# Performance work log

Hardware: AMD Instinct MI355X
Metric: run time of the kernel (lower is better)

## Reference

```python
import jax, jax.numpy as jnp
import numpy as np

DIM = 768
HEADS = 12
HEAD_DIM = DIM // HEADS
SCALE = HEAD_DIM ** -0.5


def setup_inputs() -> dict:
    key = jax.random.key(0)
    k1, k2, k3, k4 = jax.random.split(key, 4)
    x = jax.random.normal(k1, (8, 1025, DIM), dtype=jnp.float32)
    # torch nn.Linear weight layout: (out_features, in_features)
    w_qkv = jax.random.normal(k2, (3 * DIM, DIM), dtype=jnp.float32) * (DIM ** -0.5)
    w_proj = jax.random.normal(k3, (DIM, DIM), dtype=jnp.float32) * (DIM ** -0.5)
    b_proj = jax.random.normal(k4, (DIM,), dtype=jnp.float32) * 0.01
    return {"x": x, "w_qkv": w_qkv, "w_proj": w_proj, "b_proj": b_proj}


def reference(x, w_qkv, w_proj, b_proj):
    B, N, C = x.shape
    H, D = HEADS, HEAD_DIM
    # qkv: (B, N, 3C) -> (3, B, H, N, D)
    qkv = jnp.einsum('bnc,oc->bno', x, w_qkv)
    qkv = qkv.reshape(B, N, 3, H, D).transpose(2, 0, 3, 1, 4)
    q, k, v = qkv[0], qkv[1], qkv[2]
    attn = jnp.einsum('bhnd,bhmd->bhnm', q, k) * SCALE
    attn = jax.nn.softmax(attn, axis=-1)
    out = jnp.einsum('bhnm,bhmd->bhnd', attn, v)
    out = out.transpose(0, 2, 1, 3).reshape(B, N, C)
    out = jnp.einsum('bnc,oc->bno', out, w_proj) + b_proj
    return out
```

## Files before the change

kernel.cpp:

```cpp
#include <hip/hip_runtime.h>
#include <stdint.h>

#define DIMC 768
#define NSEQ 1025
#define BATCH 8
#define HEADS 12
#define HDIM 64
#define OC3 2304
#define MROWS (BATCH * NSEQ)
#define KVB 64
#define NT 17
#define QTILE 128
#define NQT 9
#define C2 0.1803368801111244f
#define OFFB (-11.541560327111707f)

typedef short bf16x8 __attribute__((ext_vector_type(8)));
typedef float f32x4 __attribute__((ext_vector_type(4)));
typedef float f32x16 __attribute__((ext_vector_type(16)));
typedef uint32_t u32x4 __attribute__((ext_vector_type(4)));

__device__ __forceinline__ uint32_t f2bf(float x) {
    uint32_t u = __builtin_bit_cast(uint32_t, x);
    return (u + 0x7fffu + ((u >> 16) & 1u)) >> 16;
}
__device__ __forceinline__ float4 ld4(const float* p) {
    return *reinterpret_cast<const float4*>(p);
}
__device__ __forceinline__ uint32_t cvtpk(float lo, float hi) {
    uint32_t r;
    asm("v_cvt_pk_bf16_f32 %0, %1, %2" : "=v"(r) : "v"(lo), "v"(hi));
    return r;
}
__device__ __forceinline__ void plswap(uint32_t& x, uint32_t& y) {
    asm volatile("v_permlane32_swap_b32 %0, %1" : "+v"(x), "+v"(y));
}
__device__ __forceinline__ void async_cp16(void* lds, const void* g) {
    __builtin_amdgcn_global_load_lds(
        (const __attribute__((address_space(1))) uint32_t*)g,
        (__attribute__((address_space(3))) uint32_t*)lds, 16, 0, 0);
}

__global__ __launch_bounds__(256) void cvt_all(const float* __restrict__ x,
                                               const float* __restrict__ wq,
                                               const float* __restrict__ wp,
                                               uint16_t* __restrict__ xb,
                                               uint16_t* __restrict__ wqb,
                                               uint16_t* __restrict__ wpb) {
    const int NX = MROWS * DIMC / 8, NQ = OC3 * DIMC / 8, NP = DIMC * DIMC / 8;
    const int i = blockIdx.x * 256 + threadIdx.x;
    const float* src;
    uint16_t* dst;
    int off;
    if (i < NX)                { src = x;  dst = xb;  off = i; }
    else if (i < NX + NQ)      { src = wq; dst = wqb; off = i - NX; }
    else if (i < NX + NQ + NP) { src = wp; dst = wpb; off = i - NX - NQ; }
    else return;
    const float4 a = ld4(src + off * 8), b = ld4(src + off * 8 + 4);
    uint4 o;
    o.x = f2bf(a.x) | (f2bf(a.y) << 16);
    o.y = f2bf(a.z) | (f2bf(a.w) << 16);
    o.z = f2bf(b.x) | (f2bf(b.y) << 16);
    o.w = f2bf(b.z) | (f2bf(b.w) << 16);
    *reinterpret_cast<uint4*>(dst + off * 8) = o;
}

template <bool OUTBF, bool BIAS>
__global__ __launch_bounds__(256) void gemm_bf16_nt(const uint16_t* __restrict__ A,
                                                    const uint16_t* __restrict__ W,
                                                    const float* __restrict__ bias,
                                                    void* __restrict__ Out,
                                                    int M, int N, int K) {
    __shared__ __align__(16) char smem[32768];
    char* const As = smem;
    char* const Ws = smem + 16384;

    const int tid = threadIdx.x;
    const int wave = tid >> 6, lane = tid & 63;
    const int l15 = lane & 15, l4 = lane >> 4;
    const int wr = wave >> 1, wc = wave & 1;
    const int m0 = blockIdx.y * 128, n0 = blockIdx.x * 128;

    f32x4 acc[4][4] = {};

    int srow[4], scol[4];
#pragma unroll
    for (int i = 0; i < 4; ++i) {
        const int X = i * 4096 + wave * 1024 + lane * 16;
        const int row = X >> 7;
        const int slot = (X & 127) >> 4;
        srow[i] = row;
        scol[i] = (slot ^ (row & 7)) << 3;
    }

    for (int kt = 0; kt < K; kt += 64) {
        __syncthreads();
#pragma unroll
        for (int i = 0; i < 4; ++i) {
            int am = m0 + srow[i];
            if (am >= M) am = M - 1;
            async_cp16(As + i * 4096 + wave * 1024,
                       A + (size_t)am * K + kt + scol[i]);
            const int wn = n0 + srow[i];
            async_cp16(Ws + i * 4096 + wave * 1024,
                       W + (size_t)wn * K + kt + scol[i]);
        }
        __syncthreads();

#pragma unroll
        for (int ch = 0; ch < 2; ++ch) {
            const int kb = (ch << 6) + (l4 << 4);
            bf16x8 af[4], bw[4];
#pragma unroll
            for (int mi = 0; mi < 4; ++mi) {
                const int row = wr * 64 + mi * 16 + l15;
                af[mi] = *(const bf16x8*)(As + (row << 7) + (kb ^ ((row & 7) << 4)));
            }
#pragma unroll
            for (int nj = 0; nj < 4; ++nj) {
                const int row = wc * 64 + nj * 16 + l15;
                bw[nj] = *(const bf16x8*)(Ws + (row << 7) + (kb ^ ((row & 7) << 4)));
            }
#pragma unroll
            for (int mi = 0; mi < 4; ++mi)
#pragma unroll
                for (int nj = 0; nj < 4; ++nj)
                    acc[mi][nj] = __builtin_amdgcn_mfma_f32_16x16x32_bf16(
                        af[mi], bw[nj], acc[mi][nj], 0, 0, 0);
        }
    }

#pragma unroll
    for (int mi = 0; mi < 4; ++mi) {
#pragma unroll
        for (int r = 0; r < 4; ++r) {
            const int m = m0 + wr * 64 + mi * 16 + l4 * 4 + r;
            if (m < M) {
#pragma unroll
                for (int nj = 0; nj < 4; ++nj) {
                    const int n = n0 + wc * 64 + nj * 16 + l15;
                    float v = acc[mi][nj][r];
                    if (BIAS) v += bias[n];
                    if (OUTBF)
                        ((uint16_t*)Out)[(size_t)m * N + n] = (uint16_t)f2bf(v);
                    else
                        ((float*)Out)[(size_t)m * N + n] = v;
                }
            }
        }
    }
}

__global__ __launch_bounds__(256) void flash_attn2(const uint16_t* __restrict__ qkv,
                                                   uint16_t* __restrict__ out) {
    const int wg = blockIdx.x;
    const int lg = (wg & 7) * 108 + (wg >> 3);
    const int qt = lg % NQT;
    const int hb = lg / NQT;
    const int h = hb % HEADS, b = hb / HEADS;

    const int tid = threadIdx.x;
    const int wave = tid >> 6, lane = tid & 63;
    const int l31 = lane & 31, lh = lane >> 5;

    __shared__ __align__(16) char smem[32768];

    const uint16_t* Kg = qkv + (size_t)b * NSEQ * OC3 + DIMC + h * HDIM;
    const uint16_t* Vg = qkv + (size_t)b * NSEQ * OC3 + 2 * DIMC + h * HDIM;

    bf16x8 qf[4];
    {
        int qrow = qt * QTILE + wave * 32 + l31;
        if (qrow > NSEQ - 1) qrow = NSEQ - 1;
        const uint16_t* Qg = qkv + (size_t)(b * NSEQ + qrow) * OC3 + h * HDIM;
#pragma unroll
        for (int ds = 0; ds < 4; ++ds)
            qf[ds] = *(const bf16x8*)(Qg + ds * 16 + lh * 8);
    }

    bf16x8 ones;
#pragma unroll
    for (int i = 0; i < 8; ++i) ones[i] = (short)0x3F80;

    uint4 va, vb;
    const int kvp = tid & 31;
    const int vd0 = (tid >> 5) * 8;

    auto stageK = [&](int kv0, char* Kb) {
#pragma unroll
        for (int i = 0; i < 2; ++i) {
            const int X = i * 4096 + wave * 1024 + lane * 16;
            const int row = X >> 7;
            const int slot = (X & 127) >> 4;
            int kvg = kv0 + row;
            if (kvg > NSEQ - 1) kvg = NSEQ - 1;
            async_cp16(Kb + i * 4096 + wave * 1024,
                       Kg + (size_t)kvg * OC3 + ((slot ^ (row & 7)) << 3));
        }
    };
    auto loadV = [&](int kv0) {
        int ka = kv0 + kvp * 2, kb2 = ka + 1;
        if (ka > NSEQ - 1) ka = NSEQ - 1;
        if (kb2 > NSEQ - 1) kb2 = NSEQ - 1;
        va = *(const uint4*)(Vg + (size_t)ka * OC3 + vd0);
        vb = *(const uint4*)(Vg + (size_t)kb2 * OC3 + vd0);
    };
    auto writeV = [&](char* Vb) {
        const uint32_t aw[4] = {va.x, va.y, va.z, va.w};
        const uint32_t bw[4] = {vb.x, vb.y, vb.z, vb.w};
#pragma unroll
        for (int t4 = 0; t4 < 4; ++t4) {
            const uint32_t lo = __builtin_amdgcn_perm(bw[t4], aw[t4], 0x05040100u);
            const uint32_t hi = __builtin_amdgcn_perm(bw[t4], aw[t4], 0x07060302u);
            const int dl = vd0 + t4 * 2, dh = dl + 1;
            *(uint32_t*)(Vb + (((dl << 7) + (kvp << 2)) ^ ((dl & 7) << 4))) = lo;
            *(uint32_t*)(Vb + (((dh << 7) + (kvp << 2)) ^ ((dh & 7) << 4))) = hi;
        }
    };

    stageK(0, smem);
    loadV(0);
    writeV(smem + 16384);
    __syncthreads();

    f32x16 o[2] = {};
    f32x16 osum = {};

    for (int t = 0; t < NT; ++t) {
        const int cur = t & 1;
        const int kv0 = t * KVB;
        char* const Kc = smem + cur * 8192;
        char* const Vc = smem + 16384 + cur * 8192;

        if (t < NT - 1) {
            stageK(kv0 + KVB, smem + (cur ^ 1) * 8192);
            loadV(kv0 + KVB);
        }

        f32x16 s[2] = {};
        __builtin_amdgcn_s_setprio(1);
#pragma unroll
        for (int kvb = 0; kvb < 2; ++kvb) {
            const int krow = kvb * 32 + l31;
            const int kbase = (krow << 7);
            const int sw = (l31 & 7) << 4;
#pragma unroll
            for (int ds = 0; ds < 4; ++ds) {
                bf16x8 kf = *(const bf16x8*)(Kc + kbase + ((ds * 32 + lh * 16) ^ sw));
                s[kvb] = __builtin_amdgcn_mfma_f32_32x32x16_bf16(kf, qf[ds], s[kvb], 0, 0, 0);
            }
        }
        __builtin_amdgcn_s_setprio(0);

        if (t == NT - 1) {
#pragma unroll
            for (int kvb = 0; kvb < 2; ++kvb)
#pragma unroll
                for (int r = 0; r < 16; ++r) {
                    const int kvg = kv0 + kvb * 32 + (r & 3) + 8 * (r >> 2) + 4 * lh;
                    if (kvg >= NSEQ) s[kvb][r] = -INFINITY;
                }
        }

#pragma unroll
        for (int kvb = 0; kvb < 2; ++kvb)
#pragma unroll
            for (int r = 0; r < 16; ++r)
                s[kvb][r] = __builtin_amdgcn_exp2f(fmaf(s[kvb][r], C2, OFFB));

        bf16x8 pa[4];
#pragma unroll
        for (int kb = 0; kb < 4; ++kb) {
            const f32x16 S = s[kb >> 1];
            const int c = (kb & 1) * 8;
            uint32_t w0 = cvtpk(S[c + 0], S[c + 1]);
            uint32_t w2 = cvtpk(S[c + 4], S[c + 5]);
            plswap(w0, w2);
            uint32_t w1 = cvtpk(S[c + 2], S[c + 3]);
            uint32_t w3 = cvtpk(S[c + 6], S[c + 7]);
            plswap(w1, w3);
            u32x4 w;
            w[0] = w0; w[1] = w1; w[2] = w2; w[3] = w3;
            pa[kb] = __builtin_bit_cast(bf16x8, w);
        }

        __builtin_amdgcn_s_setprio(1);
#pragma unroll
        for (int kb = 0; kb < 4; ++kb)
            osum = __builtin_amdgcn_mfma_f32_32x32x16_bf16(ones, pa[kb], osum, 0, 0, 0);
#pragma unroll
        for (int db = 0; db < 2; ++db) {
            const int d = db * 32 + l31;
            const int dbase = (d << 7);
            const int sw = (l31 & 7) << 4;
#pragma unroll
            for (int kb = 0; kb < 4; ++kb) {
                bf16x8 vf = *(const bf16x8*)(Vc + dbase + ((kb * 32 + lh * 16) ^ sw));
                o[db] = __builtin_amdgcn_mfma_f32_32x32x16_bf16(vf, pa[kb], o[db], 0, 0, 0);
            }
        }
        __builtin_amdgcn_s_setprio(0);

        if (t < NT - 1) {
            writeV(smem + 16384 + (cur ^ 1) * 8192);
            __syncthreads();
        }
    }

    {
        const int qrow = qt * QTILE + wave * 32 + l31;
        if (qrow < NSEQ) {
            const float inv = 1.0f / osum[0];
            uint16_t* orow = out + (size_t)(b * NSEQ + qrow) * DIMC + h * HDIM;
#pragma unroll
            for (int db = 0; db < 2; ++db)
#pragma unroll
                for (int g = 0; g < 4; ++g) {
                    const int d = db * 32 + g * 8 + lh * 4;
                    uint2 ww;
                    ww.x = cvtpk(o[db][g * 4 + 0] * inv, o[db][g * 4 + 1] * inv);
                    ww.y = cvtpk(o[db][g * 4 + 2] * inv, o[db][g * 4 + 3] * inv);
                    *(uint2*)(orow + d) = ww;
                }
        }
    }
}

extern "C" void kernel_launch(void* const* d_in, const int* in_sizes, int n_in,
                              void* d_out, int out_size, void* d_ws, size_t ws_size,
                              hipStream_t stream) {
    const float* x      = (const float*)d_in[0];
    const float* w_qkv  = (const float*)d_in[1];
    const float* w_proj = (const float*)d_in[2];
    const float* b_proj = (const float*)d_in[3];
    float* out = (float*)d_out;

    uint16_t* xb   = (uint16_t*)d_ws;
    uint16_t* wqb  = xb  + (size_t)MROWS * DIMC;
    uint16_t* wpb  = wqb + (size_t)OC3 * DIMC;
    uint16_t* qkv  = wpb + (size_t)DIMC * DIMC;
    uint16_t* attb = qkv + (size_t)MROWS * OC3;

    const dim3 blk(256);
    const int ncvt = (MROWS * DIMC + OC3 * DIMC + DIMC * DIMC) / 8;
    cvt_all<<<dim3((ncvt + 255) / 256), blk, 0, stream>>>(x, w_qkv, w_proj, xb, wqb, wpb);

    gemm_bf16_nt<true, false><<<dim3(OC3 / 128, (MROWS + 127) / 128), blk, 0, stream>>>(
        xb, wqb, nullptr, qkv, MROWS, OC3, DIMC);

    flash_attn2<<<dim3(NQT * HEADS * BATCH), blk, 0, stream>>>(qkv, attb);

    gemm_bf16_nt<false, true><<<dim3(DIMC / 128, (MROWS + 127) / 128), blk, 0, stream>>>(
        attb, wpb, b_proj, out, MROWS, DIMC, DIMC);
}
```

Baseline: 127.6 us.

## Emit head-major Q/K and transposed V from QKV GEMM epilogue

The QKV GEMM epilogue now scatters its output into per-(batch, head) Q and K buffers and a transposed V buffer laid out [bh][d][seq], instead of one interleaved qkv matrix. The attention kernel can then stage V into shared memory with the same async 16-byte copies used for K. This removes the register load, permute and LDS write path for V and the extra sync it needed. In exchange, the epilogue issues 2-byte transposed V stores strided by 1025 elements, which coalesce poorly. The V row stride is odd, so the 16-byte async reads are misaligned, and the last tile reads past the end of each row into neighbouring data, relying on masking to discard it.

Measured after the change: 139.7 us. 9.5% more time.

```diff
diff --git a/kernel.cpp b/kernel.cpp
--- a/kernel.cpp
+++ b/kernel.cpp
@@ -8,6 +8,7 @@
 #define HDIM 64
 #define OC3 2304
 #define MROWS (BATCH * NSEQ)
+#define NBH (BATCH * HEADS)
 #define KVB 64
 #define NT 17
 #define QTILE 128
@@ -65,11 +66,14 @@
     *reinterpret_cast<uint4*>(dst + off * 8) = o;
 }
 
-template <bool OUTBF, bool BIAS>
+template <bool QKVOUT, bool BIAS>
 __global__ __launch_bounds__(256) void gemm_bf16_nt(const uint16_t* __restrict__ A,
                                                     const uint16_t* __restrict__ W,
                                                     const float* __restrict__ bias,
                                                     void* __restrict__ Out,
+                                                    uint16_t* __restrict__ qh,
+                                                    uint16_t* __restrict__ kh,
+                                                    uint16_t* __restrict__ vt,
                                                     int M, int N, int K) {
     __shared__ __align__(16) char smem[32768];
     char* const As = smem;
@@ -136,28 +140,47 @@
         for (int r = 0; r < 4; ++r) {
             const int m = m0 + wr * 64 + mi * 16 + l4 * 4 + r;
             if (m < M) {
-#pragma unroll
-                for (int nj = 0; nj < 4; ++nj) {
-                    const int n = n0 + wc * 64 + nj * 16 + l15;
-                    float v = acc[mi][nj][r];
-                    if (BIAS) v += bias[n];
-                    if (OUTBF)
-                        ((uint16_t*)Out)[(size_t)m * N + n] = (uint16_t)f2bf(v);
-                    else
+                if (QKVOUT) {
+                    const int bidx = m / NSEQ;
+                    const int nq = m - bidx * NSEQ;
+#pragma unroll
+                    for (int nj = 0; nj < 4; ++nj) {
+                        const int n = n0 + wc * 64 + nj * 16 + l15;
+                        const uint16_t v = (uint16_t)f2bf(acc[mi][nj][r]);
+                        const int part = n / DIMC;
+                        const int hh = (n - part * DIMC) >> 6;
+                        const int dd = n & 63;
+                        const size_t bh = (size_t)bidx * HEADS + hh;
+                        if (part == 0)
+                            qh[(bh * NSEQ + nq) * HDIM + dd] = v;
+                        else if (part == 1)
+                            kh[(bh * NSEQ + nq) * HDIM + dd] = v;
+                        else
+                            vt[(bh * HDIM + dd) * NSEQ + nq] = v;
+                    }
+                } else {
+#pragma unroll
+                    for (int nj = 0; nj < 4; ++nj) {
+                        const int n = n0 + wc * 64 + nj * 16 + l15;
+                        float v = acc[mi][nj][r];
+                        if (BIAS) v += bias[n];
                         ((float*)Out)[(size_t)m * N + n] = v;
+                    }
                 }
             }
         }
     }
 }
 
-__global__ __launch_bounds__(256) void flash_attn2(const uint16_t* __restrict__ qkv,
+__global__ __launch_bounds__(256) void flash_attn2(const uint16_t* __restrict__ qh,
+                                                   const uint16_t* __restrict__ kh,
+                                                   const uint16_t* __restrict__ vt,
                                                    uint16_t* __restrict__ out) {
     const int wg = blockIdx.x;
     const int lg = (wg & 7) * 108 + (wg >> 3);
     const int qt = lg % NQT;
-    const int hb = lg / NQT;
-    const int h = hb % HEADS, b = hb / HEADS;
+    const int bh = lg / NQT;
+    const int h = bh % HEADS, b = bh / HEADS;
 
     const int tid = threadIdx.x;
     const int wave = tid >> 6, lane = tid & 63;
@@ -165,14 +188,14 @@
 
     __shared__ __align__(16) char smem[32768];
 
-    const uint16_t* Kg = qkv + (size_t)b * NSEQ * OC3 + DIMC + h * HDIM;
-    const uint16_t* Vg = qkv + (size_t)b * NSEQ * OC3 + 2 * DIMC + h * HDIM;
+    const uint16_t* Kh = kh + (size_t)bh * NSEQ * HDIM;
+    const uint16_t* Vt = vt + (size_t)bh * HDIM * NSEQ;
 
     bf16x8 qf[4];
     {
         int qrow = qt * QTILE + wave * 32 + l31;
         if (qrow > NSEQ - 1) qrow = NSEQ - 1;
-        const uint16_t* Qg = qkv + (size_t)(b * NSEQ + qrow) * OC3 + h * HDIM;
+        const uint16_t* Qg = qh + ((size_t)bh * NSEQ + qrow) * HDIM;
 #pragma unroll
         for (int ds = 0; ds < 4; ++ds)
             qf[ds] = *(const bf16x8*)(Qg + ds * 16 + lh * 8);
@@ -181,10 +204,6 @@
     bf16x8 ones;
 #pragma unroll
     for (int i = 0; i < 8; ++i) ones[i] = (short)0x3F80;
-
-    uint4 va, vb;
-    const int kvp = tid & 31;
-    const int vd0 = (tid >> 5) * 8;
 
     auto stageK = [&](int kv0, char* Kb) {
 #pragma unroll
@@ -195,32 +214,22 @@
             int kvg = kv0 + row;
             if (kvg > NSEQ - 1) kvg = NSEQ - 1;
             async_cp16(Kb + i * 4096 + wave * 1024,
-                       Kg + (size_t)kvg * OC3 + ((slot ^ (row & 7)) << 3));
+                       Kh + (size_t)kvg * HDIM + ((slot ^ (row & 7)) << 3));
         }
     };
-    auto loadV = [&](int kv0) {
-        int ka = kv0 + kvp * 2, kb2 = ka + 1;
-        if (ka > NSEQ - 1) ka = NSEQ - 1;
-        if (kb2 > NSEQ - 1) kb2 = NSEQ - 1;
-        va = *(const uint4*)(Vg + (size_t)ka * OC3 + vd0);
-        vb = *(const uint4*)(Vg + (size_t)kb2 * OC3 + vd0);
+    auto stageV = [&](int kv0, char* Vb) {
+#pragma unroll
+        for (int i = 0; i < 2; ++i) {
+            const int X = i * 4096 + wave * 1024 + lane * 16;
+            const int d = X >> 7;
+            const int slot = (X & 127) >> 4;
+            async_cp16(Vb + i * 4096 + wave * 1024,
+                       Vt + (size_t)d * NSEQ + kv0 + ((slot ^ (d & 7)) << 3));
+        }
     };
-    auto writeV = [&](char* Vb) {
-        const uint32_t aw[4] = {va.x, va.y, va.z, va.w};
-        const uint32_t bw[4] = {vb.x, vb.y, vb.z, vb.w};
-#pragma unroll
-        for (int t4 = 0; t4 < 4; ++t4) {
-            const uint32_t lo = __builtin_amdgcn_perm(bw[t4], aw[t4], 0x05040100u);
-            const uint32_t hi = __builtin_amdgcn_perm(bw[t4], aw[t4], 0x07060302u);
-            const int dl = vd0 + t4 * 2, dh = dl + 1;
-            *(uint32_t*)(Vb + (((dl << 7) + (kvp << 2)) ^ ((dl & 7) << 4))) = lo;
-            *(uint32_t*)(Vb + (((dh << 7) + (kvp << 2)) ^ ((dh & 7) << 4))) = hi;
-        }
-    };
 
     stageK(0, smem);
-    loadV(0);
-    writeV(smem + 16384);
+    stageV(0, smem + 16384);
     __syncthreads();
 
     f32x16 o[2] = {};
@@ -234,7 +243,7 @@
 
         if (t < NT - 1) {
             stageK(kv0 + KVB, smem + (cur ^ 1) * 8192);
-            loadV(kv0 + KVB);
+            stageV(kv0 + KVB, smem + 16384 + (cur ^ 1) * 8192);
         }
 
         f32x16 s[2] = {};
@@ -301,10 +310,7 @@
         }
         __builtin_amdgcn_s_setprio(0);
 
-        if (t < NT - 1) {
-            writeV(smem + 16384 + (cur ^ 1) * 8192);
-            __syncthreads();
-        }
+        if (t < NT - 1) __syncthreads();
     }
 
     {
@@ -335,21 +341,24 @@
     const float* b_proj = (const float*)d_in[3];
     float* out = (float*)d_out;
 
+    const size_t NHD = (size_t)NBH * NSEQ * HDIM;
     uint16_t* xb   = (uint16_t*)d_ws;
     uint16_t* wqb  = xb  + (size_t)MROWS * DIMC;
     uint16_t* wpb  = wqb + (size_t)OC3 * DIMC;
-    uint16_t* qkv  = wpb + (size_t)DIMC * DIMC;
-    uint16_t* attb = qkv + (size_t)MROWS * OC3;
+    uint16_t* qh   = wpb + (size_t)DIMC * DIMC;
+    uint16_t* kh   = qh + NHD;
+    uint16_t* vt   = kh + NHD;
+    uint16_t* attb = vt + NHD;
 
     const dim3 blk(256);
     const int ncvt = (MROWS * DIMC + OC3 * DIMC + DIMC * DIMC) / 8;
     cvt_all<<<dim3((ncvt + 255) / 256), blk, 0, stream>>>(x, w_qkv, w_proj, xb, wqb, wpb);
 
     gemm_bf16_nt<true, false><<<dim3(OC3 / 128, (MROWS + 127) / 128), blk, 0, stream>>>(
-        xb, wqb, nullptr, qkv, MROWS, OC3, DIMC);
-
-    flash_attn2<<<dim3(NQT * HEADS * BATCH), blk, 0, stream>>>(qkv, attb);
+        xb, wqb, nullptr, nullptr, qh, kh, vt, MROWS, OC3, DIMC);
+
+    flash_attn2<<<dim3(NQT * HEADS * BATCH), blk, 0, stream>>>(qh, kh, vt, attb);
 
     gemm_bf16_nt<false, true><<<dim3(DIMC / 128, (MROWS + 127) / 128), blk, 0, stream>>>(
-        attb, wpb, b_proj, out, MROWS, DIMC, DIMC);
-}
+        attb, wpb, b_proj, out, nullptr, nullptr, nullptr, MROWS, DIMC, DIMC);
+}
```
